# Kernel optimization log

Measured on AMD Instinct MI355X. Metric: run time of the kernel, lower is better.

## Reference

```python
import jax, jax.numpy as jnp
import numpy as np

N_NODE = 100000
HIDDEN = 128
BATCH = 4096
SESS_LEN = 50


def setup_inputs() -> dict:
    key = jax.random.key(0)
    k1, k2, k3, k4, k5 = jax.random.split(key, 5)
    return {
        "item_embedding": jax.random.normal(k1, (N_NODE, HIDDEN), dtype=jnp.float32),
        "items": jax.random.randint(k2, (BATCH, SESS_LEN), 0, N_NODE, dtype=jnp.int64),
        "A": jax.random.uniform(k3, (BATCH, BATCH), dtype=jnp.float32),
        "D": jax.random.uniform(k4, (BATCH, BATCH), dtype=jnp.float32),
        "target_embedding": jax.random.normal(k5, (BATCH, 1, 2 * HIDDEN), dtype=jnp.float32),
    }


def reference(item_embedding, items, A, D, target_embedding):
    # Gather per-session item embeddings: (batch, sess_len, hidden)
    seq_h = item_embedding[items]
    # Sum over session positions -> (batch, hidden)
    relation_emb = jnp.sum(seq_h, axis=1)
    # DA = D @ A, then propagate: (batch, batch) @ (batch, hidden)
    DA = jnp.matmul(D, A)
    relation_emb = jnp.matmul(DA, relation_emb)
    # Row-wise L2 normalization (torch.norm(dim=-1))
    norm = jnp.linalg.norm(relation_emb, axis=-1, keepdims=True)
    return relation_emb / norm
```

## Files before the change

kernel.cpp:

```cpp
#include <hip/hip_runtime.h>
#include <hip/hip_bf16.h>

#define BATCH   4096
#define HIDDEN  128
#define SESS    50
#define KTOT    4096
#define NB      ((size_t)BATCH * HIDDEN)

#define BK        512
#define KCH       16
#define NTILES    (KTOT / BK)
#define ROWSTRIDE 2064
#define BUFSZ     (16 * ROWSTRIDE)

typedef __bf16 bf16x8 __attribute__((ext_vector_type(8)));
typedef __bf16 bf16x4 __attribute__((ext_vector_type(4)));
typedef float  f32x4  __attribute__((ext_vector_type(4)));

__device__ __forceinline__ f32x4 mfma_bf16(bf16x8 a, bf16x8 b, f32x4 c) {
    return __builtin_amdgcn_mfma_f32_16x16x32_bf16(a, b, c, 0, 0, 0);
}

__device__ __forceinline__ void gload16(const void* g, void* l) {
    __builtin_amdgcn_global_load_lds(
        (const __attribute__((address_space(1))) void*)g,
        (__attribute__((address_space(3))) void*)l, 16, 0, 0);
}


__global__ __launch_bounds__(256)
void gather_sum_kernel(const float* __restrict__ emb,
                       const int* __restrict__ items32,
                       __bf16* __restrict__ ETp) {
    __shared__ int sidx[4][SESS];
    const int t  = threadIdx.x;
    const int b0 = blockIdx.x * 4;
    const bool is64 = (items32[1] | items32[3] | items32[5] | items32[7] |
                       items32[9] | items32[11] | items32[13] | items32[15]) == 0;
    if (t < 4 * SESS) {
        const int w_ = t / SESS, s_ = t % SESS;
        sidx[w_][s_] = is64
            ? (int)((const long long*)items32)[(long)(b0 + w_) * SESS + s_]
            : items32[(b0 + w_) * SESS + s_];
    }
    __syncthreads();
    const int w    = t >> 6;
    const int lane = t & 63;
    const int c    = lane & 31;
    const int h    = lane >> 5;
    f32x4 acc = {0.f, 0.f, 0.f, 0.f};
#pragma unroll
    for (int i = 0; i < 25; ++i) {
        acc += *(const f32x4*)(emb + (long)sidx[w][h + 2 * i] * HIDDEN + c * 4);
    }
#pragma unroll
    for (int j = 0; j < 4; ++j) acc[j] += __shfl_xor(acc[j], 32, 64);
    if (h == 0) {
        const int b  = b0 + w;
        const int h0 = c * 4;
        const long pb = ((long)(b >> 3) << 10) + (b & 7) + ((h0 >> 4) << 7);
#pragma unroll
        for (int j = 0; j < 4; ++j)
            ETp[pb + ((h0 & 15) + j) * 8] = (__bf16)acc[j];
    }
}

template <int PHASE>
__global__ __launch_bounds__(256, 1)
void gemm_mfma_kernel(const float* __restrict__ X,
                      const __bf16* __restrict__ Bpk,
                      __bf16* __restrict__ TTp,
                      float* __restrict__ out) {
    __shared__ __align__(16) char lds[2 * BUFSZ];
    const int tid  = threadIdx.x;
    const int w    = tid >> 6;
    const int lane = tid & 63;
    const int lo   = lane & 15;
    const int quad = lane >> 4;
    const int rowBase = blockIdx.x * 16;

    const float* xb = X + (size_t)(rowBase + 4 * w) * KTOT + lane * 4;

#define STAGE(t_, b_) do {                                                   \
    _Pragma("unroll")                                                        \
    for (int r_ = 0; r_ < 4; ++r_) {                                         \
        _Pragma("unroll")                                                    \
        for (int p_ = 0; p_ < 2; ++p_) {                                     \
            gload16(xb + (size_t)r_ * KTOT + (t_) * BK + p_ * 256,           \
                    lds + (b_) * BUFSZ + (4 * w + r_) * ROWSTRIDE +          \
                        p_ * 1024);                                          \
        }                                                                    \
    }                                                                        \
} while (0)

    f32x4 acc0 = {0.f, 0.f, 0.f, 0.f};
    f32x4 acc1 = {0.f, 0.f, 0.f, 0.f};
    const __bf16* bq = Bpk + quad * 1024 + (2 * w) * 128 + lo * 8;

#define KTILE(t_, cur_) do {                                                 \
    const char* As = lds + (cur_) * BUFSZ + lo * ROWSTRIDE + quad * 32;      \
    const __bf16* bp = bq + (size_t)(t_) * KCH * 4096;                       \
    _Pragma("unroll")                                                        \
    for (int ks = 0; ks < KCH; ++ks) {                                       \
        const f32x4 a0 = *(const f32x4*)(As + ks * 128);                     \
        const f32x4 a1 = *(const f32x4*)(As + ks * 128 + 16);                \
        const bf16x8 b0 = *(const bf16x8*)(bp + (size_t)ks * 4096);          \
        const bf16x8 b1 = *(const bf16x8*)(bp + (size_t)ks * 4096 + 128);    \
        bf16x8 af;                                                           \
        af[0] = (__bf16)a0[0]; af[1] = (__bf16)a0[1];                        \
        af[2] = (__bf16)a0[2]; af[3] = (__bf16)a0[3];                        \
        af[4] = (__bf16)a1[0]; af[5] = (__bf16)a1[1];                        \
        af[6] = (__bf16)a1[2]; af[7] = (__bf16)a1[3];                        \
        acc0 = mfma_bf16(af, b0, acc0);                                      \
        acc1 = mfma_bf16(af, b1, acc1);                                      \
    }                                                                        \
} while (0)

    STAGE(0, 0);
    for (int t = 0; t < NTILES - 1; ++t) {
        const int cur = t & 1;
        STAGE(t + 1, cur ^ 1);
        asm volatile("s_waitcnt vmcnt(8)" ::: "memory");
        __builtin_amdgcn_s_barrier();
        __builtin_amdgcn_sched_barrier(0);
        KTILE(t, cur);
        __builtin_amdgcn_s_barrier();
        __builtin_amdgcn_sched_barrier(0);
    }
    {
        asm volatile("s_waitcnt vmcnt(0)" ::: "memory");
        __builtin_amdgcn_s_barrier();
        __builtin_amdgcn_sched_barrier(0);
        KTILE(NTILES - 1, (NTILES - 1) & 1);
        __builtin_amdgcn_s_barrier();
        __builtin_amdgcn_sched_barrier(0);
    }
#undef KTILE
#undef STAGE

    if (PHASE == 1) {
        __bf16* tb = TTp + ((rowBase >> 3) + (quad >> 1)) * 1024 + lo * 8 +
                     (quad & 1) * 4;
        bf16x4 p0, p1;
#pragma unroll
        for (int r = 0; r < 4; ++r) {
            p0[r] = (__bf16)acc0[r];
            p1[r] = (__bf16)acc1[r];
        }
        *(bf16x4*)(tb + (2 * w) * 128)     = p0;
        *(bf16x4*)(tb + (2 * w + 1) * 128) = p1;
    } else {
        float (*Cs)[136] = (float (*)[136])lds;
#pragma unroll
        for (int r = 0; r < 4; ++r) {
            Cs[quad * 4 + r][(2 * w) * 16 + lo]     = acc0[r];
            Cs[quad * 4 + r][(2 * w + 1) * 16 + lo] = acc1[r];
        }
        __syncthreads();
        const int row = tid >> 4;
        const int cg  = tid & 15;
        const f32x4 c0 = *(const f32x4*)&Cs[row][cg * 8];
        const f32x4 c1 = *(const f32x4*)&Cs[row][cg * 8 + 4];
        float sq = c0[0] * c0[0] + c0[1] * c0[1] + c0[2] * c0[2] +
                   c0[3] * c0[3] + c1[0] * c1[0] + c1[1] * c1[1] +
                   c1[2] * c1[2] + c1[3] * c1[3];
#pragma unroll
        for (int m = 1; m < 16; m <<= 1) sq += __shfl_xor(sq, m, 64);
        const float s = rsqrtf(sq);
        float* op = out + (size_t)(rowBase + row) * HIDDEN + cg * 8;
        f32x4 o0, o1;
#pragma unroll
        for (int j = 0; j < 4; ++j) { o0[j] = c0[j] * s; o1[j] = c1[j] * s; }
        *(f32x4*)(op)     = o0;
        *(f32x4*)(op + 4) = o1;
    }
}

extern "C" void kernel_launch(void* const* d_in, const int* in_sizes, int n_in,
                              void* d_out, int out_size, void* d_ws, size_t ws_size,
                              hipStream_t stream) {
    const float* emb   = (const float*)d_in[0];
    const int*   items = (const int*)d_in[1];
    const float* A     = (const float*)d_in[2];
    const float* D     = (const float*)d_in[3];
    float* out = (float*)d_out;

    __bf16* ETp = (__bf16*)d_ws;
    __bf16* TTp = ETp + NB;

    gather_sum_kernel<<<BATCH / 4, 256, 0, stream>>>(emb, items, ETp);
    gemm_mfma_kernel<1><<<BATCH / 16, 256, 0, stream>>>(A, ETp, TTp, nullptr);
    gemm_mfma_kernel<2><<<BATCH / 16, 256, 0, stream>>>(D, TTp, nullptr, out);
}
```

Before: 227.0 us.

## Stage B operand through LDS with swizzled layout and triple-buffered pipeline

The GEMM kernels now load the packed bf16 B operand into LDS through async global-to-LDS copies instead of reading it directly from global memory in the inner loop. The A operand is staged with an XOR swizzle to avoid bank conflicts, and the K tile shrinks to 128 with three buffers so two tiles are kept in flight. The producer layouts (gather output and phase-1 output) are rewritten to match the new swizzled B layout. This aims to cut global-latency stalls on B loads and LDS bank conflicts, at the cost of more LDS traffic and more barriers per K step.

```diff
diff --git a/kernel.cpp b/kernel.cpp
--- a/kernel.cpp
+++ b/kernel.cpp
@@ -7,11 +7,11 @@
 #define KTOT    4096
 #define NB      ((size_t)BATCH * HIDDEN)
 
-#define BK        512
-#define KCH       16
-#define NTILES    (KTOT / BK)
-#define ROWSTRIDE 2064
-#define BUFSZ     (16 * ROWSTRIDE)
+#define BK      128
+#define NTILES  (KTOT / BK)
+#define ABYTES  8192
+#define BBYTES  32768
+#define BUF     (ABYTES + BBYTES)
 
 typedef __bf16 bf16x8 __attribute__((ext_vector_type(8)));
 typedef __bf16 bf16x4 __attribute__((ext_vector_type(4)));
@@ -56,12 +56,16 @@
 #pragma unroll
     for (int j = 0; j < 4; ++j) acc[j] += __shfl_xor(acc[j], 32, 64);
     if (h == 0) {
-        const int b  = b0 + w;
-        const int h0 = c * 4;
-        const long pb = ((long)(b >> 3) << 10) + (b & 7) + ((h0 >> 4) << 7);
-#pragma unroll
-        for (int j = 0; j < 4; ++j)
-            ETp[pb + ((h0 & 15) + j) * 8] = (__bf16)acc[j];
+        const int  b     = b0 + w;
+        const long chunk = b >> 3;
+        const int  swz   = (int)((chunk & 3) << 4);
+        char* basep = (char*)ETp + chunk * 2048 + (b & 7) * 2;
+        const int hi4 = (c >> 2) * 256;
+#pragma unroll
+        for (int j = 0; j < 4; ++j) {
+            const int hl = 4 * (c & 3) + j;
+            *(__bf16*)(basep + ((hi4 + hl * 16) ^ swz)) = (__bf16)acc[j];
+        }
     }
 }
 
@@ -71,7 +75,7 @@
                       const __bf16* __restrict__ Bpk,
                       __bf16* __restrict__ TTp,
                       float* __restrict__ out) {
-    __shared__ __align__(16) char lds[2 * BUFSZ];
+    __shared__ __align__(16) char lds[3 * BUF];
     const int tid  = threadIdx.x;
     const int w    = tid >> 6;
     const int lane = tid & 63;
@@ -79,77 +83,92 @@
     const int quad = lane >> 4;
     const int rowBase = blockIdx.x * 16;
 
-    const float* xb = X + (size_t)(rowBase + 4 * w) * KTOT + lane * 4;
-
-#define STAGE(t_, b_) do {                                                   \
+#define STAGE(t_, dst_) do {                                                 \
     _Pragma("unroll")                                                        \
-    for (int r_ = 0; r_ < 4; ++r_) {                                         \
-        _Pragma("unroll")                                                    \
-        for (int p_ = 0; p_ < 2; ++p_) {                                     \
-            gload16(xb + (size_t)r_ * KTOT + (t_) * BK + p_ * 256,           \
-                    lds + (b_) * BUFSZ + (4 * w + r_) * ROWSTRIDE +          \
-                        p_ * 1024);                                          \
-        }                                                                    \
+    for (int oi_ = 0; oi_ < 2; ++oi_) {                                      \
+        const int o_    = 2 * w + oi_;                                       \
+        const int rloc_ = 2 * o_ + (lane >> 5);                              \
+        gload16((const char*)X +                                             \
+                    ((size_t)(rowBase + rloc_) * KTOT + (size_t)(t_) * BK) * 4 + \
+                    (((lane & 31) * 16) ^ ((rloc_ & 7) << 4)),               \
+                (dst_) + o_ * 1024);                                         \
+    }                                                                        \
+    _Pragma("unroll")                                                        \
+    for (int bi_ = 0; bi_ < 8; ++bi_) {                                      \
+        const int i_ = 8 * w + bi_;                                          \
+        gload16((const char*)Bpk + (size_t)(t_) * BBYTES + i_ * 1024 +       \
+                    lane * 16,                                               \
+                (dst_) + ABYTES + i_ * 1024);                                \
     }                                                                        \
 } while (0)
 
     f32x4 acc0 = {0.f, 0.f, 0.f, 0.f};
     f32x4 acc1 = {0.f, 0.f, 0.f, 0.f};
-    const __bf16* bq = Bpk + quad * 1024 + (2 * w) * 128 + lo * 8;
-
-#define KTILE(t_, cur_) do {                                                 \
-    const char* As = lds + (cur_) * BUFSZ + lo * ROWSTRIDE + quad * 32;      \
-    const __bf16* bp = bq + (size_t)(t_) * KCH * 4096;                       \
+
+    const int akey = (lo & 7) << 4;
+    const int bswz = quad << 4;
+    const int bc0  = (int)(((2 * w) * 256 + lo * 16) ^ bswz);
+    const int bc1  = (int)(((2 * w + 1) * 256 + lo * 16) ^ bswz);
+
+#define KTILE(cb_) do {                                                      \
+    const char* Ar_ = (cb_) + lo * 512;                                      \
+    const char* Bb_ = (cb_) + ABYTES + quad * 2048;                          \
     _Pragma("unroll")                                                        \
-    for (int ks = 0; ks < KCH; ++ks) {                                       \
-        const f32x4 a0 = *(const f32x4*)(As + ks * 128);                     \
-        const f32x4 a1 = *(const f32x4*)(As + ks * 128 + 16);                \
-        const bf16x8 b0 = *(const bf16x8*)(bp + (size_t)ks * 4096);          \
-        const bf16x8 b1 = *(const bf16x8*)(bp + (size_t)ks * 4096 + 128);    \
-        bf16x8 af;                                                           \
-        af[0] = (__bf16)a0[0]; af[1] = (__bf16)a0[1];                        \
-        af[2] = (__bf16)a0[2]; af[3] = (__bf16)a0[3];                        \
-        af[4] = (__bf16)a1[0]; af[5] = (__bf16)a1[1];                        \
-        af[6] = (__bf16)a1[2]; af[7] = (__bf16)a1[3];                        \
-        acc0 = mfma_bf16(af, b0, acc0);                                      \
-        acc1 = mfma_bf16(af, b1, acc1);                                      \
+    for (int ks_ = 0; ks_ < 4; ++ks_) {                                      \
+        const f32x4 a0_ =                                                    \
+            *(const f32x4*)(Ar_ + ((ks_ * 128 + quad * 32) ^ akey));         \
+        const f32x4 a1_ =                                                    \
+            *(const f32x4*)(Ar_ + ((ks_ * 128 + quad * 32 + 16) ^ akey));    \
+        const bf16x8 b0_ = *(const bf16x8*)(Bb_ + ks_ * 8192 + bc0);         \
+        const bf16x8 b1_ = *(const bf16x8*)(Bb_ + ks_ * 8192 + bc1);         \
+        bf16x8 af_;                                                          \
+        af_[0] = (__bf16)a0_[0]; af_[1] = (__bf16)a0_[1];                    \
+        af_[2] = (__bf16)a0_[2]; af_[3] = (__bf16)a0_[3];                    \
+        af_[4] = (__bf16)a1_[0]; af_[5] = (__bf16)a1_[1];                    \
+        af_[6] = (__bf16)a1_[2]; af_[7] = (__bf16)a1_[3];                    \
+        acc0 = mfma_bf16(af_, b0_, acc0);                                    \
+        acc1 = mfma_bf16(af_, b1_, acc1);                                    \
     }                                                                        \
 } while (0)
 
-    STAGE(0, 0);
-    for (int t = 0; t < NTILES - 1; ++t) {
-        const int cur = t & 1;
-        STAGE(t + 1, cur ^ 1);
-        asm volatile("s_waitcnt vmcnt(8)" ::: "memory");
+    STAGE(0, lds);
+    STAGE(1, lds + BUF);
+
+    char* cb = lds;
+    char* sb = lds + 2 * BUF;
+    for (int t = 0; t < NTILES; ++t) {
+        if (t + 2 < NTILES) STAGE(t + 2, sb);
+        if (t < NTILES - 2)
+            asm volatile("s_waitcnt vmcnt(20)" ::: "memory");
+        else if (t == NTILES - 2)
+            asm volatile("s_waitcnt vmcnt(10)" ::: "memory");
+        else
+            asm volatile("s_waitcnt vmcnt(0)" ::: "memory");
         __builtin_amdgcn_s_barrier();
         __builtin_amdgcn_sched_barrier(0);
-        KTILE(t, cur);
+        KTILE(cb);
         __builtin_amdgcn_s_barrier();
         __builtin_amdgcn_sched_barrier(0);
-    }
-    {
-        asm volatile("s_waitcnt vmcnt(0)" ::: "memory");
-        __builtin_amdgcn_s_barrier();
-        __builtin_amdgcn_sched_barrier(0);
-        KTILE(NTILES - 1, (NTILES - 1) & 1);
-        __builtin_amdgcn_s_barrier();
-        __builtin_amdgcn_sched_barrier(0);
+        cb += BUF; if (cb == lds + 3 * BUF) cb = lds;
+        sb += BUF; if (sb == lds + 3 * BUF) sb = lds;
     }
 #undef KTILE
 #undef STAGE
 
     if (PHASE == 1) {
-        __bf16* tb = TTp + ((rowBase >> 3) + (quad >> 1)) * 1024 + lo * 8 +
-                     (quad & 1) * 4;
+        const long chunk = (rowBase >> 3) + (quad >> 1);
+        const int  swz   = (int)((chunk & 3) << 4);
+        char* tb = (char*)TTp + chunk * 2048 + (quad & 1) * 8;
         bf16x4 p0, p1;
 #pragma unroll
         for (int r = 0; r < 4; ++r) {
             p0[r] = (__bf16)acc0[r];
             p1[r] = (__bf16)acc1[r];
         }
-        *(bf16x4*)(tb + (2 * w) * 128)     = p0;
-        *(bf16x4*)(tb + (2 * w + 1) * 128) = p1;
+        *(bf16x4*)(tb + (((2 * w) * 256 + lo * 16) ^ swz))     = p0;
+        *(bf16x4*)(tb + (((2 * w + 1) * 256 + lo * 16) ^ swz)) = p1;
     } else {
+        __syncthreads();
         float (*Cs)[136] = (float (*)[136])lds;
 #pragma unroll
         for (int r = 0; r < 4; ++r) {
```

After: 207.9 us (median of 2 runs). -8.4%, faster.
